# Performance work log

Measured on AMD Instinct MI355X. Metric: run time of the kernel, lower is better.

Reference implementation:

```python
import jax, jax.numpy as jnp
import numpy as np

VOXEL_SIZE = jnp.array([0.2, 0.2, 0.2], dtype=jnp.float32)  # (vx, vy, vz)
SCALE_MULT = 3.0
K = 64            # max_neighbors
CHUNK = 4096
EPS = 1e-8


def setup_inputs() -> dict:
    key = jax.random.key(0)
    k1, k2, k3, k4, k5 = jax.random.split(key, 5)
    M, N = 49152, 8192
    pc_range = jnp.array([-51.2, -51.2, -5.0, 51.2, 51.2, 3.0], dtype=jnp.float32)
    # voxel coords: (b, z, y, x) with grid sizes matching pc_range / voxel_size
    b = jnp.zeros((M, 1), dtype=jnp.int32)
    z = jax.random.randint(k1, (M, 1), 0, 40, dtype=jnp.int32)
    y = jax.random.randint(k2, (M, 1), 0, 512, dtype=jnp.int32)
    x = jax.random.randint(k3, (M, 1), 0, 512, dtype=jnp.int32)
    voxel_coords = jnp.concatenate([b, z, y, x], axis=1)
    # Gaussian means uniform inside the point-cloud range, positive scales ~[0.1, 1.1] m
    lo, hi = pc_range[:3], pc_range[3:]
    mu = lo + jax.random.uniform(k4, (N, 3), dtype=jnp.float32) * (hi - lo)
    scale = 0.1 + jax.random.uniform(k5, (N, 3), dtype=jnp.float32)
    return {"voxel_coords": voxel_coords, "mu": mu, "scale": scale, "pc_range": pc_range}


def _voxel_centers(voxel_coords, pc_range):
    # coords are (b, z, y, x) -> centers (cx, cy, cz)
    xyz_idx = voxel_coords[:, jnp.array([3, 2, 1])].astype(jnp.float32)
    return pc_range[:3][None, :] + (xyz_idx + 0.5) * VOXEL_SIZE[None, :]


def reference(voxel_coords, mu, scale, pc_range):
    centers = _voxel_centers(voxel_coords, pc_range)          # [M,3]
    inv = 1.0 / (scale * scale + EPS)                          # [N,3]
    radii_sq = (SCALE_MULT ** 2) * jnp.sum(scale * scale, -1)  # [N]
    mu_inv = mu * inv                                          # [N,3]
    mu_term = jnp.sum(mu * mu_inv, axis=-1)                    # [N]

    Qs = centers.reshape(-1, CHUNK, 3)  # M assumed divisible by CHUNK

    def per_chunk(Q):
        # expanded Mahalanobis-like sq distance: sum_d (q_d - mu_d)^2 / (s_d^2+eps)
        d2 = (Q * Q) @ inv.T - 2.0 * (Q @ mu_inv.T) + mu_term[None, :]  # [C,N]
        score = jnp.where(d2 <= radii_sq[None, :], -d2, -jnp.inf)
        top_score, top_idx = jax.lax.top_k(score, K)                     # [C,K]
        valid = jnp.isfinite(top_score)
        idx = jnp.where(valid, top_idx, -1)
        w = jnp.where(valid, -top_score, 0.0)
        return idx, w, valid

    idxs, ws, masks = jax.lax.map(per_chunk, Qs)
    M = centers.shape[0]
    neighbor_indices = idxs.reshape(M, K).astype(jnp.int64)
    neighbor_weights = ws.reshape(M, K)
    neighbor_masks = masks.reshape(M, K)
    return centers, neighbor_indices, neighbor_weights, neighbor_masks
```

## Files before the change

kernel.cpp:

```cpp
#include <hip/hip_runtime.h>

#define KTOP 64
#define GX   32
#define NCELL (GX*GX)
#define CSF  3.2f
#define X0F  -51.2f
#define GCAP 384
#define QCAP 128
#define CAPQ 80
#define CH   (GCAP/64)

#define BAR(x) asm volatile("" : "+v"(x))

__device__ inline bool cell_hits(int cx, int cy, double mux, double muy, double reach2)
{
    const double lx = (double)X0F + (double)cx * (double)CSF - 1e-3;
    const double hx = lx + (double)CSF + 2e-3;
    const double ly = (double)X0F + (double)cy * (double)CSF - 1e-3;
    const double hy = ly + (double)CSF + 2e-3;
    double dx = 0.0, dy = 0.0;
    if (mux < lx) dx = lx - mux; else if (mux > hx) dx = mux - hx;
    if (muy < ly) dy = ly - muy; else if (muy > hy) dy = muy - hy;
    return dx*dx + dy*dy <= reach2;
}

__device__ inline void q_center(int ix, int iy, int iz, float pc0, float pc1, float pc2,
                                float& qx, float& qy, float& qz)
{
    float tx = ((float)ix + 0.5f) * 0.2f; BAR(tx);
    float ty = ((float)iy + 0.5f) * 0.2f; BAR(ty);
    float tz = ((float)iz + 0.5f) * 0.2f; BAR(tz);
    qx = pc0 + tx;  qy = pc1 + ty;  qz = pc2 + tz;
}

__device__ inline int q_cell(float qx, float qy)
{
    int cx = (int)floorf((qx - X0F) * (1.0f / CSF));
    int cy = (int)floorf((qy - X0F) * (1.0f / CSF));
    cx = cx < 0 ? 0 : (cx > GX-1 ? GX-1 : cx);
    cy = cy < 0 ? 0 : (cy > GX-1 ? GX-1 : cy);
    return cy * GX + cx;
}

__device__ inline unsigned long long pack_key(float d2, int g)
{
    unsigned int b = __float_as_uint(d2);
    unsigned int k = (b & 0x80000000u) ? ~b : (b | 0x80000000u);
    return ((unsigned long long)k << 32) | (unsigned int)g;
}

__device__ inline float unpack_d2(unsigned long long key)
{
    unsigned int k = (unsigned int)(key >> 32);
    unsigned int b = (k & 0x80000000u) ? (k & 0x7FFFFFFFu) : ~k;
    return __uint_as_float(b);
}

__global__ __launch_bounds__(256)
void k_init(int4* __restrict__ cnts4, int ncnt4,
            float4* __restrict__ idxb4, float4* __restrict__ wb4,
            float4* __restrict__ mb4, int nf4)
{
    const int gtid = blockIdx.x * 256 + threadIdx.x;
    const int S = gridDim.x * 256;
    for (int i = gtid; i < ncnt4; i += S) cnts4[i] = make_int4(0, 0, 0, 0);
    const float4 mi = make_float4(-1.f, -1.f, -1.f, -1.f);
    const float4 zz = make_float4(0.f, 0.f, 0.f, 0.f);
    for (int i = gtid; i < nf4; i += S) idxb4[i] = mi;
    for (int i = gtid; i < nf4; i += S) wb4[i] = zz;
    for (int i = gtid; i < nf4; i += S) mb4[i] = zz;
}

__global__ __launch_bounds__(256)
void k_build(const float* __restrict__ mu, const float* __restrict__ scale,
             const int* __restrict__ vox, const float* __restrict__ pcr,
             float* __restrict__ params,
             int* __restrict__ gcnt, int* __restrict__ qcnt,
             unsigned short* __restrict__ entries, float4* __restrict__ qinfo,
             float* __restrict__ out, int N, int M, int GSB)
{
    const int b = blockIdx.x;
    if (b < GSB) {
        const int t = b * 256 + threadIdx.x;
        const int g = t >> 5, slot = t & 31;
        if (g >= N) return;
        const float s0 = scale[3*g+0], s1 = scale[3*g+1], s2 = scale[3*g+2];
        const float m0 = mu[3*g+0],    m1 = mu[3*g+1],    m2 = mu[3*g+2];

        if (slot == 0) {
            float s0s = s0 * s0; BAR(s0s);
            float s1s = s1 * s1; BAR(s1s);
            float s2s = s2 * s2; BAR(s2s);
            float d0 = s0s + 1e-8f;
            float d1 = s1s + 1e-8f;
            float dd2 = s2s + 1e-8f;
            float i0 = 1.0f / d0;
            float i1 = 1.0f / d1;
            float i2 = 1.0f / dd2;
            float mi0 = m0 * i0; BAR(mi0);
            float mi1 = m1 * i1; BAR(mi1);
            float mi2 = m2 * i2; BAR(mi2);
            float p0 = m0 * mi0; BAR(p0);
            float p1 = m1 * mi1; BAR(p1);
            float p2 = m2 * mi2; BAR(p2);
            float mt = (p0 + p1) + p2;
            float rs = (s0s + s1s) + s2s;
            float r2 = 9.0f * rs;
            *(float4*)&params[(size_t)g*8]     = make_float4(i0, i1, i2, mi0);
            *(float4*)&params[(size_t)g*8 + 4] = make_float4(mi1, mi2, mt, r2);
        }

        const double ss0 = (double)s0 * (double)s0 + 1e-8;
        const double ss1 = (double)s1 * (double)s1 + 1e-8;
        const double ss2 = (double)s2 * (double)s2 + 1e-8;
        double smax = ss0 > ss1 ? ss0 : ss1; smax = smax > ss2 ? smax : ss2;
        const double sum = ss0 + ss1 + ss2;
        const double reach2 = 9.0 * smax * sum * 1.0005 + 0.5;
        const double reach = sqrt(reach2);
        const double mux = (double)m0, muy = (double)m1;
        int cx0 = (int)floor((mux - reach - (double)X0F) / (double)CSF);
        int cx1 = (int)floor((mux + reach - (double)X0F) / (double)CSF);
        int cy0 = (int)floor((muy - reach - (double)X0F) / (double)CSF);
        int cy1 = (int)floor((muy + reach - (double)X0F) / (double)CSF);
        cx0 = cx0 < 0 ? 0 : cx0;  cy0 = cy0 < 0 ? 0 : cy0;
        cx1 = cx1 > GX-1 ? GX-1 : cx1;  cy1 = cy1 > GX-1 ? GX-1 : cy1;
        const int w = cx1 - cx0 + 1, h = cy1 - cy0 + 1;
        if (slot >= w * h) return;
        const int cx = cx0 + slot % w;
        const int cy = cy0 + slot / w;
        if (cell_hits(cx, cy, mux, muy, reach2)) {
            const int cell = cy * GX + cx;
            int pos = atomicAdd(&gcnt[cell], 1);
            if (pos < GCAP) entries[(size_t)cell * GCAP + pos] = (unsigned short)g;
        }
    } else {
        const int q = (b - GSB) * 256 + threadIdx.x;
        if (q >= M) return;
        int4 c = ((const int4*)vox)[q];
        float qx, qy, qz;
        q_center(c.w, c.z, c.y, pcr[0], pcr[1], pcr[2], qx, qy, qz);
        out[3*(size_t)q + 0] = qx;
        out[3*(size_t)q + 1] = qy;
        out[3*(size_t)q + 2] = qz;
        const int cell = q_cell(qx, qy);
        int pos = atomicAdd(&qcnt[cell], 1);
        if (pos < QCAP) {
            float4 qi; qi.x = qx; qi.y = qy; qi.z = qz; qi.w = __int_as_float(q);
            qinfo[(size_t)cell * QCAP + pos] = qi;
        }
    }
}

__global__ __launch_bounds__(64)
void k_append(const float* __restrict__ params,
              const unsigned short* __restrict__ entries, const int* __restrict__ gcnt,
              const float4* __restrict__ qinfo, const int* __restrict__ qcnt,
              int* __restrict__ ccnt, unsigned long long* __restrict__ cand)
{
    const int cell = blockIdx.x;
    const int half = blockIdx.y;
    int L = gcnt[cell]; L = L < GCAP ? L : GCAP;
    int nq = qcnt[cell]; nq = nq < QCAP ? nq : QCAP;
    if (nq == 0 || L == 0) return;

    const int l = threadIdx.x;
    const unsigned short* ebase = entries + (size_t)cell * GCAP;
    const float4* qbase = qinfo + (size_t)cell * QCAP;

    float4 pa[CH], pb[CH];
    int    gg[CH];
    bool   has[CH];
    #pragma unroll
    for (int c = 0; c < CH; ++c) {
        const int idx = c * 64 + l;
        has[c] = (idx < L);
        gg[c]  = has[c] ? ebase[idx] : 0;
        pa[c]  = *(const float4*)&params[(size_t)gg[c] * 8];
        pb[c]  = *(const float4*)&params[(size_t)gg[c] * 8 + 4];
    }

    for (int j = half; j < nq; j += 2) {
        const float4 qi = qbase[j];
        const float qx = qi.x, qy = qi.y, qz = qi.z;
        const int qid = __float_as_int(qi.w);
        float qx2 = qx * qx; BAR(qx2);
        float qy2 = qy * qy; BAR(qy2);
        float qz2 = qz * qz; BAR(qz2);

        unsigned long long* cq = cand + (size_t)qid * CAPQ;
        int ofs = 0;
        #pragma unroll
        for (int c = 0; c < CH; ++c) {
            float t1 = __builtin_fmaf(qz2, pa[c].z, __builtin_fmaf(qy2, pa[c].y, qx2 * pa[c].x));
            float t2 = __builtin_fmaf(qz,  pb[c].y, __builtin_fmaf(qy,  pb[c].x, qx  * pa[c].w));
            const float d2v = (t1 - 2.0f * t2) + pb[c].z;
            const bool pass = has[c] && (d2v <= pb[c].w);
            const unsigned long long pm = __ballot(pass);
            if (pass) {
                const int pos = ofs + __popcll(pm & ((1ull << l) - 1ull));
                if (pos < CAPQ) cq[pos] = pack_key(d2v, gg[c]);
            }
            ofs += __popcll(pm);
        }
        if (l == 0) ccnt[qid] = ofs;
    }
}

__global__ __launch_bounds__(256)
void k_rank(const unsigned long long* __restrict__ cand, const int* __restrict__ ccnt,
            float* __restrict__ out, int M)
{
    const int t = blockIdx.x * 256 + threadIdx.x;
    const int q = t / CAPQ;
    const int p = t - q * CAPQ;
    if (q >= M) return;
    int cnt = ccnt[q]; cnt = cnt < CAPQ ? cnt : CAPQ;
    if (p >= cnt) return;
    const unsigned long long* cb = cand + (size_t)q * CAPQ;
    const unsigned long long v = cb[p];
    int r = 0;
    for (int i = 0; i < cnt; ++i) r += (cb[i] < v) ? 1 : 0;
    if (r < KTOP) {
        float* idxb = out + 3 * (size_t)M;
        float* wb   = idxb + (size_t)M * KTOP;
        float* mb   = wb   + (size_t)M * KTOP;
        const size_t o = (size_t)q * KTOP + r;
        idxb[o] = (float)(unsigned int)(v & 0xFFFFFFFFull);
        wb[o]   = unpack_d2(v);
        mb[o]   = 1.0f;
    }
}

extern "C" void kernel_launch(void* const* d_in, const int* in_sizes, int n_in,
                              void* d_out, int out_size, void* d_ws, size_t ws_size,
                              hipStream_t stream)
{
    const int*   vox   = (const int*)d_in[0];
    const float* mu    = (const float*)d_in[1];
    const float* scale = (const float*)d_in[2];
    const float* pcr   = (const float*)d_in[3];
    float* out = (float*)d_out;

    const int M = in_sizes[0] / 4;
    const int N = in_sizes[1] / 3;

    char* ws = (char*)d_ws;
    size_t o = 0;
    int* cnts = (int*)(ws + o);                          o += (((size_t)(2*NCELL) + M) * 4 + 255) & ~(size_t)255;
    float* params = (float*)(ws + o);                    o += ((size_t)N * 32 + 255) & ~(size_t)255;
    unsigned short* entries = (unsigned short*)(ws + o); o += ((size_t)NCELL * GCAP * 2 + 255) & ~(size_t)255;
    float4* qinfo = (float4*)(ws + o);                   o += ((size_t)NCELL * QCAP * 16 + 255) & ~(size_t)255;
    unsigned long long* cand = (unsigned long long*)(ws + o); o += ((size_t)M * CAPQ * 8 + 255) & ~(size_t)255;
    int* gcnt = cnts;
    int* qcnt = cnts + NCELL;
    int* ccnt = cnts + 2 * NCELL;

    const int GSB = (N * 32 + 255) / 256;
    const int QB  = (M + 255) / 256;

    float* idxb = out + 3 * (size_t)M;
    float* wb   = idxb + (size_t)M * KTOP;
    float* mb   = wb   + (size_t)M * KTOP;
    const int ncnt4 = (2 * NCELL + M) / 4;
    const int nf4   = (M * KTOP) / 4;

    hipLaunchKernelGGL(k_init, dim3(2048), dim3(256), 0, stream,
                       (int4*)cnts, ncnt4, (float4*)idxb, (float4*)wb, (float4*)mb, nf4);
    hipLaunchKernelGGL(k_build, dim3(GSB + QB), dim3(256), 0, stream,
                       mu, scale, vox, pcr, params, gcnt, qcnt, entries, qinfo, out, N, M, GSB);
    hipLaunchKernelGGL(k_append, dim3(NCELL, 2), dim3(64), 0, stream,
                       params, entries, gcnt, qinfo, qcnt, ccnt, cand);
    hipLaunchKernelGGL(k_rank, dim3((M * CAPQ + 255) / 256), dim3(256), 0, stream,
                       cand, ccnt, out, M);
}
```

Measured before the change: 128.2 us.

## Fuse candidate ranking into cell scan kernel and drop global candidate buffer

The candidate append and rank kernels are merged, so each query's candidates go into a shared-memory list and are ranked in place by the same wavefront. It then writes the top-K slots plus the -1/0 padding directly. This removes the global cand/ccnt buffers, the full-output init pass and one kernel launch, and raises the per-cell query parallelism from 2 to 4 blocks. The cost is a serial O(cnt^2) rank inside one 64-thread block per query, and params are reloaded by more blocks. Queries whose cell has no gaussians are now handled by the block loop and get padding written.

```diff
diff --git a/kernel.cpp b/kernel.cpp
--- a/kernel.cpp
+++ b/kernel.cpp
@@ -9,6 +9,7 @@
 #define QCAP 128
 #define CAPQ 80
 #define CH   (GCAP/64)
+#define PAR  4
 
 #define BAR(x) asm volatile("" : "+v"(x))
 
@@ -56,19 +57,10 @@
     return __uint_as_float(b);
 }
 
-__global__ __launch_bounds__(256)
-void k_init(int4* __restrict__ cnts4, int ncnt4,
-            float4* __restrict__ idxb4, float4* __restrict__ wb4,
-            float4* __restrict__ mb4, int nf4)
-{
-    const int gtid = blockIdx.x * 256 + threadIdx.x;
-    const int S = gridDim.x * 256;
-    for (int i = gtid; i < ncnt4; i += S) cnts4[i] = make_int4(0, 0, 0, 0);
-    const float4 mi = make_float4(-1.f, -1.f, -1.f, -1.f);
-    const float4 zz = make_float4(0.f, 0.f, 0.f, 0.f);
-    for (int i = gtid; i < nf4; i += S) idxb4[i] = mi;
-    for (int i = gtid; i < nf4; i += S) wb4[i] = zz;
-    for (int i = gtid; i < nf4; i += S) mb4[i] = zz;
+__global__ __launch_bounds__(1024)
+void k_zero(int* __restrict__ cnts)
+{
+    cnts[blockIdx.x * 1024 + threadIdx.x] = 0;
 }
 
 __global__ __launch_bounds__(256)
@@ -129,7 +121,7 @@
         const int cx = cx0 + slot % w;
         const int cy = cy0 + slot / w;
         if (cell_hits(cx, cy, mux, muy, reach2)) {
-            const int cell = cy * GX + cx;
+            const int cell = cy*GX + cx;
             int pos = atomicAdd(&gcnt[cell], 1);
             if (pos < GCAP) entries[(size_t)cell * GCAP + pos] = (unsigned short)g;
         }
@@ -152,16 +144,18 @@
 }
 
 __global__ __launch_bounds__(64)
-void k_append(const float* __restrict__ params,
-              const unsigned short* __restrict__ entries, const int* __restrict__ gcnt,
-              const float4* __restrict__ qinfo, const int* __restrict__ qcnt,
-              int* __restrict__ ccnt, unsigned long long* __restrict__ cand)
-{
+void k_scan(const float* __restrict__ params,
+            const unsigned short* __restrict__ entries, const int* __restrict__ gcnt,
+            const float4* __restrict__ qinfo, const int* __restrict__ qcnt,
+            float* __restrict__ out, int M)
+{
+    __shared__ unsigned long long lst[CAPQ];
+
     const int cell = blockIdx.x;
-    const int half = blockIdx.y;
+    const int part = blockIdx.y;
     int L = gcnt[cell]; L = L < GCAP ? L : GCAP;
     int nq = qcnt[cell]; nq = nq < QCAP ? nq : QCAP;
-    if (nq == 0 || L == 0) return;
+    if (part >= nq) return;
 
     const int l = threadIdx.x;
     const unsigned short* ebase = entries + (size_t)cell * GCAP;
@@ -179,7 +173,11 @@
         pb[c]  = *(const float4*)&params[(size_t)gg[c] * 8 + 4];
     }
 
-    for (int j = half; j < nq; j += 2) {
+    float* idxb = out + 3 * (size_t)M;
+    float* wb   = idxb + (size_t)M * KTOP;
+    float* mb   = wb   + (size_t)M * KTOP;
+
+    for (int j = part; j < nq; j += PAR) {
         const float4 qi = qbase[j];
         const float qx = qi.x, qy = qi.y, qz = qi.z;
         const int qid = __float_as_int(qi.w);
@@ -187,7 +185,6 @@
         float qy2 = qy * qy; BAR(qy2);
         float qz2 = qz * qz; BAR(qz2);
 
-        unsigned long long* cq = cand + (size_t)qid * CAPQ;
         int ofs = 0;
         #pragma unroll
         for (int c = 0; c < CH; ++c) {
@@ -198,36 +195,31 @@
             const unsigned long long pm = __ballot(pass);
             if (pass) {
                 const int pos = ofs + __popcll(pm & ((1ull << l) - 1ull));
-                if (pos < CAPQ) cq[pos] = pack_key(d2v, gg[c]);
+                if (pos < CAPQ) lst[pos] = pack_key(d2v, gg[c]);
             }
             ofs += __popcll(pm);
         }
-        if (l == 0) ccnt[qid] = ofs;
-    }
-}
-
-__global__ __launch_bounds__(256)
-void k_rank(const unsigned long long* __restrict__ cand, const int* __restrict__ ccnt,
-            float* __restrict__ out, int M)
-{
-    const int t = blockIdx.x * 256 + threadIdx.x;
-    const int q = t / CAPQ;
-    const int p = t - q * CAPQ;
-    if (q >= M) return;
-    int cnt = ccnt[q]; cnt = cnt < CAPQ ? cnt : CAPQ;
-    if (p >= cnt) return;
-    const unsigned long long* cb = cand + (size_t)q * CAPQ;
-    const unsigned long long v = cb[p];
-    int r = 0;
-    for (int i = 0; i < cnt; ++i) r += (cb[i] < v) ? 1 : 0;
-    if (r < KTOP) {
-        float* idxb = out + 3 * (size_t)M;
-        float* wb   = idxb + (size_t)M * KTOP;
-        float* mb   = wb   + (size_t)M * KTOP;
-        const size_t o = (size_t)q * KTOP + r;
-        idxb[o] = (float)(unsigned int)(v & 0xFFFFFFFFull);
-        wb[o]   = unpack_d2(v);
-        mb[o]   = 1.0f;
+        __syncthreads();
+
+        const int cnt = ofs < CAPQ ? ofs : CAPQ;
+        const size_t base = (size_t)qid * KTOP;
+
+        for (int p = l; p < cnt; p += 64) {
+            const unsigned long long v = lst[p];
+            int r = 0;
+            for (int i = 0; i < cnt; ++i) r += (lst[i] < v) ? 1 : 0;
+            if (r < KTOP) {
+                idxb[base + r] = (float)(unsigned int)(v & 0xFFFFFFFFull);
+                wb[base + r]   = unpack_d2(v);
+                mb[base + r]   = 1.0f;
+            }
+        }
+        if (l >= cnt) {
+            idxb[base + l] = -1.0f;
+            wb[base + l]   = 0.0f;
+            mb[base + l]   = 0.0f;
+        }
+        __syncthreads();
     }
 }
 
@@ -246,30 +238,19 @@
 
     char* ws = (char*)d_ws;
     size_t o = 0;
-    int* cnts = (int*)(ws + o);                          o += (((size_t)(2*NCELL) + M) * 4 + 255) & ~(size_t)255;
+    int* cnts = (int*)(ws + o);                          o += (2 * NCELL * 4 + 255) & ~(size_t)255;
     float* params = (float*)(ws + o);                    o += ((size_t)N * 32 + 255) & ~(size_t)255;
     unsigned short* entries = (unsigned short*)(ws + o); o += ((size_t)NCELL * GCAP * 2 + 255) & ~(size_t)255;
     float4* qinfo = (float4*)(ws + o);                   o += ((size_t)NCELL * QCAP * 16 + 255) & ~(size_t)255;
-    unsigned long long* cand = (unsigned long long*)(ws + o); o += ((size_t)M * CAPQ * 8 + 255) & ~(size_t)255;
     int* gcnt = cnts;
     int* qcnt = cnts + NCELL;
-    int* ccnt = cnts + 2 * NCELL;
 
     const int GSB = (N * 32 + 255) / 256;
     const int QB  = (M + 255) / 256;
 
-    float* idxb = out + 3 * (size_t)M;
-    float* wb   = idxb + (size_t)M * KTOP;
-    float* mb   = wb   + (size_t)M * KTOP;
-    const int ncnt4 = (2 * NCELL + M) / 4;
-    const int nf4   = (M * KTOP) / 4;
-
-    hipLaunchKernelGGL(k_init, dim3(2048), dim3(256), 0, stream,
-                       (int4*)cnts, ncnt4, (float4*)idxb, (float4*)wb, (float4*)mb, nf4);
+    hipLaunchKernelGGL(k_zero, dim3(2), dim3(1024), 0, stream, cnts);
     hipLaunchKernelGGL(k_build, dim3(GSB + QB), dim3(256), 0, stream,
                        mu, scale, vox, pcr, params, gcnt, qcnt, entries, qinfo, out, N, M, GSB);
-    hipLaunchKernelGGL(k_append, dim3(NCELL, 2), dim3(64), 0, stream,
-                       params, entries, gcnt, qinfo, qcnt, ccnt, cand);
-    hipLaunchKernelGGL(k_rank, dim3((M * CAPQ + 255) / 256), dim3(256), 0, stream,
-                       cand, ccnt, out, M);
-}
+    hipLaunchKernelGGL(k_scan, dim3(NCELL, PAR), dim3(64), 0, stream,
+                       params, entries, gcnt, qinfo, qcnt, out, M);
+}
```

Result: faster. 106.9 us (-16.6%).
